# Performance work log

Measured on AMD Instinct MI355X. Metric: run time of the kernel, lower is better.

## Reference

```python
import jax, jax.numpy as jnp
import numpy as np

# B batch, N seq (n_vec), V vocab, D model dim, H heads, DH head dim,
# L depth, WS window size, R landmark rank, C classes
B, N, V, D, H, DH, L, WS, R, C = 4, 4096, 512, 512, 8, 64, 4, 128, 256, 10
FF = 4 * D
SCALE = DH ** -0.5


def _ln(t, g, b, eps=1e-5):
    mu = jnp.mean(t, axis=-1, keepdims=True)
    var = jnp.var(t, axis=-1, keepdims=True)
    return (t - mu) * jax.lax.rsqrt(var + eps) * g + b


def setup_inputs():
    key = jax.random.key(0)
    ks = iter(jax.random.split(key, 16))

    def w(shape, s=0.02):
        return (jax.random.normal(next(ks), shape) * s).astype(jnp.float32)

    return dict(
        x=jax.random.randint(next(ks), (B, N), 0, V, dtype=jnp.int32),
        tok_emb=w((V, D)), pos_emb=w((N, D)),
        ln1_g=jnp.ones((L, D), jnp.float32), ln1_b=jnp.zeros((L, D), jnp.float32),
        Wq=w((L, D, H * DH)), Wkv=w((L, D, 2 * H * DH)), Wp=w((L, DH, R)),
        lln_g=jnp.ones((L, DH), jnp.float32), lln_b=jnp.zeros((L, DH), jnp.float32),
        gln_g=jnp.ones((L, DH), jnp.float32), gln_b=jnp.zeros((L, DH), jnp.float32),
        Wo=w((L, H * DH, D)), bo=jnp.zeros((L, D), jnp.float32),
        ln2_g=jnp.ones((L, D), jnp.float32), ln2_b=jnp.zeros((L, D), jnp.float32),
        W1=w((L, D, FF)), b1=jnp.zeros((L, FF), jnp.float32),
        W2=w((L, FF, D)), b2=jnp.zeros((L, D), jnp.float32),
        lnf_g=jnp.ones((D,), jnp.float32), lnf_b=jnp.zeros((D,), jnp.float32),
        Wlog=w((D, V)), blog=jnp.zeros((V,), jnp.float32),
        Wfin=w((N * V, C), 0.005), bfin=jnp.zeros((C,), jnp.float32),
    )


def _forward(x, tok_emb, pos_emb, ln1_g, ln1_b, Wq, Wkv, Wp, lln_g, lln_b,
             gln_g, gln_b, Wo, bo, ln2_g, ln2_b, W1, b1, W2, b2,
             lnf_g, lnf_b, Wlog, blog, Wfin, bfin):
    h = tok_emb[x] + pos_emb[None, :, :]  # [B,N,D]
    nw = N // WS
    for l in range(L):
        # ---- PreNorm Long-Short attention ----
        y = _ln(h, ln1_g[l], ln1_b[l])
        q = (y @ Wq[l]).reshape(B, N, H, DH).transpose(0, 2, 1, 3) * SCALE  # [B,H,N,DH]
        kv = (y @ Wkv[l]).reshape(B, N, 2, H, DH).transpose(2, 0, 3, 1, 4)
        k, v = kv[0], kv[1]  # [B,H,N,DH]
        # dynamic low-rank landmark projection: softmax over the sequence dim
        p = jax.nn.softmax(jnp.einsum('bhnd,dr->bhnr', k, Wp[l]), axis=2)
        gk = _ln(jnp.einsum('bhnr,bhnd->bhrd', p, k), gln_g[l], gln_b[l])  # [B,H,R,DH]
        gv = _ln(jnp.einsum('bhnr,bhnd->bhrd', p, v), gln_g[l], gln_b[l])
        # DualLN on the short-range (local window) keys/values
        lk = _ln(k, lln_g[l], lln_b[l]).reshape(B, H, nw, WS, DH)
        lv = _ln(v, lln_g[l], lln_b[l]).reshape(B, H, nw, WS, DH)
        lq = q.reshape(B, H, nw, WS, DH)
        sim_l = jnp.einsum('bhnwd,bhnxd->bhnwx', lq, lk)  # [B,H,nw,WS,WS]
        sim_g = jnp.einsum('bhnwd,bhrd->bhnwr', lq, gk)   # [B,H,nw,WS,R]
        attn = jax.nn.softmax(jnp.concatenate([sim_l, sim_g], axis=-1), axis=-1)
        a_l, a_g = attn[..., :WS], attn[..., WS:]
        o = (jnp.einsum('bhnwx,bhnxd->bhnwd', a_l, lv)
             + jnp.einsum('bhnwr,bhrd->bhnwd', a_g, gv))
        o = o.reshape(B, H, N, DH).transpose(0, 2, 1, 3).reshape(B, N, H * DH)
        h = h + o @ Wo[l] + bo[l]
        # ---- PreNorm FeedForward ----
        y = _ln(h, ln2_g[l], ln2_b[l])
        h = h + jax.nn.gelu(y @ W1[l] + b1[l]) @ W2[l] + b2[l]
    logits = _ln(h, lnf_g, lnf_b) @ Wlog + blog  # [B,N,V]
    # FLATTEN pooling head (dropout is identity in eval mode)
    return logits.reshape(B, N * V) @ Wfin + bfin  # [B,C]


def reference(x, tok_emb, pos_emb, ln1_g, ln1_b, Wq, Wkv, Wp, lln_g, lln_b,
              gln_g, gln_b, Wo, bo, ln2_g, ln2_b, W1, b1, W2, b2,
              lnf_g, lnf_b, Wlog, blog, Wfin, bfin):
    return _forward(x, tok_emb, pos_emb, ln1_g, ln1_b, Wq, Wkv, Wp, lln_g, lln_b,
                    gln_g, gln_b, Wo, bo, ln2_g, ln2_b, W1, b1, W2, b2,
                    lnf_g, lnf_b, Wlog, blog, Wfin, bfin)
```

## Files before the change

kernel.cpp:

```cpp
#include <hip/hip_runtime.h>
#include <hip/hip_bf16.h>

typedef unsigned short u16;
typedef __attribute__((ext_vector_type(8))) short short8;
typedef __attribute__((ext_vector_type(4))) float floatx4;

#define FLAG_GELU   1
#define FLAG_ACC    2
#define FLAG_NN     4
#define FLAG_CF32   8
#define FLAG_ATOMIC 16

__device__ __forceinline__ float bf2f(u16 u){
  union { unsigned u; float f; } c; c.u = ((unsigned)u)<<16; return c.f;
}
__device__ __forceinline__ u16 f2bf(float f){
  union { float f; unsigned u; } c; c.f = f;
  unsigned r = (c.u + 0x7fffu + ((c.u>>16)&1u))>>16;
  return (u16)r;
}
__device__ __forceinline__ float rdin(const void* base, long long idx, int flagv){
  return flagv ? ((const float*)base)[idx] : bf2f(((const u16*)base)[idx]);
}
__device__ __forceinline__ float fast_gelu(float x){
  float u = 0.7978845608028654f*(x + 0.044715f*x*x*x);
  float e = __expf(2.f*u);
  float t = 1.f - 2.f/(e+1.f);
  return 0.5f*x*(1.f+t);
}

__global__ void detect_kernel(const void* tok, int* flag){
  __shared__ int cnt;
  if(threadIdx.x==0) cnt=0;
  __syncthreads();
  float v = fabsf(bf2f(((const u16*)tok)[threadIdx.x]));
  int bad = (v < 1e3f) ? 0 : 1;
  atomicAdd(&cnt, bad);
  __syncthreads();
  if(threadIdx.x==0) *flag = (cnt>0) ? 1 : 0;
}

__global__ void cvtT_kernel(const void* src, long long off0, long long zstride, u16* __restrict__ dst,
    long long dzstride, int K, int N, const int* flag){
  __shared__ float tl[32][33];
  int fl = *flag;
  int k0 = blockIdx.x*32, n0 = blockIdx.y*32;
  long long base = off0 + (long long)blockIdx.z*zstride;
  for(int i=threadIdx.y;i<32;i+=8){
    long long idx = base + (long long)(k0+i)*N + n0 + threadIdx.x;
    tl[i][threadIdx.x] = fl ? ((const float*)src)[idx] : bf2f(((const u16*)src)[idx]);
  }
  __syncthreads();
  u16* dz = dst + (long long)blockIdx.z*dzstride;
  for(int i=threadIdx.y;i<32;i+=8)
    dz[(long long)(n0+i)*K + k0 + threadIdx.x] = f2bf(tl[threadIdx.x][i]);
}

__global__ void transposeB_kernel(const u16* __restrict__ in, u16* __restrict__ out,
    long long izs0, long long izs1, int zd, long long ozstride, int ldin, int ldout){
  __shared__ u16 tl[32][33];
  int z = blockIdx.z; int z0 = z/zd, z1 = z - z0*zd;
  const u16* ip = in + z0*izs0 + z1*izs1;
  u16* op = out + (long long)z*ozstride;
  int r0 = blockIdx.x*32, c0 = blockIdx.y*32;
  for(int i=threadIdx.y;i<32;i+=8)
    tl[i][threadIdx.x] = ip[(long long)(r0+i)*ldin + c0 + threadIdx.x];
  __syncthreads();
  for(int i=threadIdx.y;i<32;i+=8)
    op[(long long)(c0+i)*ldout + r0 + threadIdx.x] = tl[threadIdx.x][i];
}

__global__ __launch_bounds__(256) void zerof_kernel(float* p, int n){
  int i = blockIdx.x*256 + threadIdx.x;
  if(i<n) p[i]=0.f;
}

struct GemmP {
  const u16* A; const u16* B; float* Cf; u16* Ch;
  const void* bias; int biasOff; const int* dflag;
  int K, lda, ldb, ldc;
  long long sA0,sA1,sA2,sB0,sB1,sB2,sC0,sC1,sC2;
  int d0,d1; float alpha; int flags; int ksplit;
};

__global__ __launch_bounds__(256) void gemm_kernel(GemmP p){
  __shared__ __align__(16) u16 As[64][40];
  __shared__ __align__(16) u16 Bs[64][40];
  int z = blockIdx.z;
  int i0 = z / p.d0; int rem = z - i0*p.d0; int i1 = rem / p.d1; int i2 = rem - i1*p.d1;
  const u16* A  = p.A + i0*p.sA0 + i1*p.sA1 + i2*p.sA2;
  const u16* Bp = p.B + i0*p.sB0 + i1*p.sB1 + i2*p.sB2;
  long long cb = i0*p.sC0 + i1*p.sC1 + i2*p.sC2;
  int kbeg = 0, kend = p.K;
  if(p.ksplit){ kbeg = i1*p.ksplit; kend = kbeg + p.ksplit; }
  int m0 = blockIdx.x*64, n0 = blockIdx.y*64;
  int t = threadIdx.x, lane = t&63, wave = t>>6;
  int wm = (wave>>1)*32, wn = (wave&1)*32;
  int quad = lane>>4, l16 = lane&15;
  floatx4 zero4 = {0.f,0.f,0.f,0.f};
  floatx4 acc00=zero4, acc01=zero4, acc10=zero4, acc11=zero4;
  int sr = t>>2, sc = (t&3)*8;
  int bkr = t>>3, bnc = (t&7)*8;
  bool nn = (p.flags & FLAG_NN);
  for(int k0=kbeg;k0<kend;k0+=32){
    uint4 av = *(const uint4*)(A + (long long)(m0+sr)*p.lda + (k0+sc));
    uint4 bv;
    if(nn) bv = *(const uint4*)(Bp + (long long)(k0+bkr)*p.ldb + (n0+bnc));
    else   bv = *(const uint4*)(Bp + (long long)(n0+sr)*p.ldb + (k0+sc));
    *(uint4*)&As[sr][sc] = av;
    if(nn){
      u16 tmp[8]; *(uint4*)tmp = bv;
      #pragma unroll
      for(int j=0;j<8;j++) Bs[bnc+j][bkr] = tmp[j];
    } else {
      *(uint4*)&Bs[sr][sc] = bv;
    }
    __syncthreads();
    short8 a0 = *(const short8*)&As[wm+l16][quad*8];
    short8 a1 = *(const short8*)&As[wm+16+l16][quad*8];
    short8 b0 = *(const short8*)&Bs[wn+l16][quad*8];
    short8 b1 = *(const short8*)&Bs[wn+16+l16][quad*8];
    acc00 = __builtin_amdgcn_mfma_f32_16x16x32_bf16(a0,b0,acc00,0,0,0);
    acc01 = __builtin_amdgcn_mfma_f32_16x16x32_bf16(a0,b1,acc01,0,0,0);
    acc10 = __builtin_amdgcn_mfma_f32_16x16x32_bf16(a1,b0,acc10,0,0,0);
    acc11 = __builtin_amdgcn_mfma_f32_16x16x32_bf16(a1,b1,acc11,0,0,0);
    __syncthreads();
  }
  int flagv = p.bias ? *p.dflag : 0;
  #pragma unroll
  for(int mi=0;mi<2;mi++){
    #pragma unroll
    for(int ni=0;ni<2;ni++){
      floatx4 a = (mi==0)?((ni==0)?acc00:acc01):((ni==0)?acc10:acc11);
      int cg = n0 + wn + ni*16 + l16;
      float bv_ = p.bias ? rdin(p.bias, (long long)p.biasOff + cg, flagv) : 0.f;
      #pragma unroll
      for(int e=0;e<4;e++){
        int rg = m0 + wm + mi*16 + quad*4 + e;
        float v = a[e]*p.alpha + bv_;
        if(p.flags & FLAG_GELU) v = fast_gelu(v);
        long long ci = cb + (long long)rg*p.ldc + cg;
        if(p.flags & FLAG_ATOMIC){
          atomicAdd(&p.Cf[ci], v);
        } else if(p.flags & FLAG_CF32){
          float o2 = v; if(p.flags&FLAG_ACC) o2 += p.Cf[ci];
          p.Cf[ci] = o2;
        } else {
          float o2 = v; if(p.flags&FLAG_ACC) o2 += bf2f(p.Ch[ci]);
          p.Ch[ci] = f2bf(o2);
        }
      }
    }
  }
}

struct Gemm128P {
  const u16* A; const u16* B; float* Cf; u16* Ch;
  const void* bias; int biasOff; const int* dflag;
  int K, lda, ldb, ldc; float alpha; int flags;
};

template<int BM>
__global__ __launch_bounds__(512) void gemm2ph_kernel(Gemm128P p){
  constexpr int NA   = BM/64;
  constexpr int HH   = BM/2;
  constexpr int MI   = HH/16;
  constexpr int ABUF = BM*64;
  constexpr int LDSZ = (BM==256) ? 69632 : 49152;
  __shared__ __align__(16) u16 lds[LDSZ];
  u16* As = lds;
  u16* Bs = lds + 2*ABUF;
  int m0 = blockIdx.x*BM, n0 = blockIdx.y*256;
  int t = threadIdx.x, lane = t&63, wave = t>>6;
  int quad = lane>>4, l16 = lane&15;
  int wr = wave>>2, wc = wave&3;
  int rowA = t>>3, colk = (t&7)*8;
  const u16* Asrc[NA];
  const u16* Bsrc[4];
  #pragma unroll
  for(int q=0;q<NA;q++) Asrc[q] = p.A + (long long)(m0 + q*64 + rowA)*p.lda + colk;
  #pragma unroll
  for(int q=0;q<4;q++)  Bsrc[q] = p.B + (long long)(n0 + q*64 + rowA)*p.ldb + colk;
  int nk = p.K >> 6;
  floatx4 acc[MI][4] = {};

  auto stage = [&](int buf, int k0){
    #pragma unroll
    for(int q=0;q<NA;q++)
      __builtin_amdgcn_global_load_lds(
        (const __attribute__((address_space(1))) unsigned int*)(Asrc[q] + k0),
        (__attribute__((address_space(3))) unsigned int*)(As + buf*ABUF + q*4096 + wave*512),
        16, 0, 0);
    #pragma unroll
    for(int q=0;q<4;q++)
      __builtin_amdgcn_global_load_lds(
        (const __attribute__((address_space(1))) unsigned int*)(Bsrc[q] + k0),
        (__attribute__((address_space(3))) unsigned int*)(Bs + buf*16384 + q*4096 + wave*512),
        16, 0, 0);
  };

  stage(0, 0);
  __syncthreads();
  for(int kt=0; kt<nk; ++kt){
    int cur = kt&1;
    if(kt+1 < nk) stage(cur^1, (kt+1)*64);
    const u16* Ab = As + cur*ABUF;
    const u16* Bb = Bs + cur*16384;
    #pragma unroll
    for(int ks=0; ks<2; ks++){
      short8 a[MI], b[4];
      #pragma unroll
      for(int i=0;i<MI;i++)
        a[i] = *(const short8*)&Ab[(wr*HH + i*16 + l16)*64 + ks*32 + quad*8];
      #pragma unroll
      for(int j=0;j<4;j++)
        b[j] = *(const short8*)&Bb[(wc*64 + j*16 + l16)*64 + ks*32 + quad*8];
      #pragma unroll
      for(int i=0;i<MI;i++)
        #pragma unroll
        for(int j=0;j<4;j++)
          acc[i][j] = __builtin_amdgcn_mfma_f32_16x16x32_bf16(a[i], b[j], acc[i][j],0,0,0);
    }
    __syncthreads();
  }

  int flagv = p.bias ? *p.dflag : 0;
  if(!(p.flags & FLAG_CF32)){
    u16* Ct = lds + wave*(HH*68);
    #pragma unroll
    for(int j=0;j<4;j++){
      int cg = n0 + wc*64 + j*16 + l16;
      float bv_ = p.bias ? rdin(p.bias, (long long)p.biasOff + cg, flagv) : 0.f;
      #pragma unroll
      for(int i=0;i<MI;i++){
        #pragma unroll
        for(int e=0;e<4;e++){
          float v = acc[i][j][e]*p.alpha + bv_;
          if(p.flags & FLAG_GELU) v = fast_gelu(v);
          Ct[(i*16 + quad*4 + e)*68 + j*16 + l16] = f2bf(v);
        }
      }
    }
    int rsub = lane>>3, csub = (lane&7)*8;
    #pragma unroll
    for(int rr=0; rr<HH/8; rr++){
      int row = rr*8 + rsub;
      uint4 v = *(const uint4*)&Ct[row*68 + csub];
      *(uint4*)(p.Ch + (long long)(m0 + wr*HH + row)*p.ldc + (n0 + wc*64 + csub)) = v;
    }
  } else {
    #pragma unroll
    for(int j=0;j<4;j++){
      int cg = n0 + wc*64 + j*16 + l16;
      float bv_ = p.bias ? rdin(p.bias, (long long)p.biasOff + cg, flagv) : 0.f;
      #pragma unroll
      for(int i=0;i<MI;i++){
        #pragma unroll
        for(int e=0;e<4;e++){
          int rg = m0 + wr*HH + i*16 + quad*4 + e;
          float v = acc[i][j][e]*p.alpha + bv_;
          if(p.flags & FLAG_GELU) v = fast_gelu(v);
          long long ci = (long long)rg*p.ldc + cg;
          float o2 = v; if(p.flags&FLAG_ACC) o2 += p.Cf[ci];
          p.Cf[ci] = o2;
        }
      }
    }
  }
}

struct AttnP {
  const u16* q;
  const u16* k;
  const u16* gk;
  const u16* vT;
  const u16* gvT;
  u16* o;
};

__global__ __launch_bounds__(256) void attn_kernel(AttnP p){
  __shared__ __align__(16) u16 S[32*392];
  __shared__ float ssum[32];
  const int SST = 392;
  int qb = blockIdx.x;
  int bh = blockIdx.y;
  int b = bh>>3, hh = bh&7;
  int w = qb>>2;
  int t = threadIdx.x, lane = t&63, wave = t>>6;
  int quad = lane>>4, l16 = lane&15;
  int mbase = qb*32;
  short8 aq[2][2];
  #pragma unroll
  for(int mt=0;mt<2;mt++)
    #pragma unroll
    for(int kc=0;kc<2;kc++)
      aq[mt][kc] = *(const short8*)(p.q + ((long long)b*4096 + mbase + mt*16 + l16)*512 + hh*64 + kc*32 + quad*8);
  #pragma unroll
  for(int i=0;i<6;i++){
    int ct = wave*6 + i;
    short8 bf0, bf1;
    if(ct<8){
      const u16* kr = p.k + ((long long)b*4096 + w*128 + ct*16 + l16)*1024 + hh*64;
      bf0 = *(const short8*)(kr + quad*8);
      bf1 = *(const short8*)(kr + 32 + quad*8);
    } else {
      const u16* gr = p.gk + ((long long)bh*256 + (ct-8)*16 + l16)*64;
      bf0 = *(const short8*)(gr + quad*8);
      bf1 = *(const short8*)(gr + 32 + quad*8);
    }
    #pragma unroll
    for(int mt=0;mt<2;mt++){
      floatx4 acc = {0.f,0.f,0.f,0.f};
      acc = __builtin_amdgcn_mfma_f32_16x16x32_bf16(aq[mt][0], bf0, acc,0,0,0);
      acc = __builtin_amdgcn_mfma_f32_16x16x32_bf16(aq[mt][1], bf1, acc,0,0,0);
      #pragma unroll
      for(int e=0;e<4;e++)
        S[(mt*16 + quad*4 + e)*SST + ct*16 + l16] = f2bf(acc[e]);
    }
  }
  __syncthreads();
  {
    int r = t>>3, seg = t&7;
    u16* Srow = S + r*SST + seg*48;
    u16 buf[48];
    #pragma unroll
    for(int it=0; it<6; it++)
      *(uint4*)(buf + it*8) = *(const uint4*)(Srow + it*8);
    float mmax = -3.4e38f;
    #pragma unroll
    for(int j=0;j<48;j++) mmax = fmaxf(mmax, bf2f(buf[j]));
    mmax = fmaxf(mmax, __shfl_xor(mmax, 1));
    mmax = fmaxf(mmax, __shfl_xor(mmax, 2));
    mmax = fmaxf(mmax, __shfl_xor(mmax, 4));
    float s = 0.f;
    #pragma unroll
    for(int j=0;j<48;j++){ float e_ = __expf(bf2f(buf[j]) - mmax); s += e_; buf[j] = f2bf(e_); }
    #pragma unroll
    for(int it=0; it<6; it++)
      *(uint4*)(Srow + it*8) = *(const uint4*)(buf + it*8);
    s += __shfl_xor(s, 1);
    s += __shfl_xor(s, 2);
    s += __shfl_xor(s, 4);
    if(seg==0) ssum[r] = 1.f/s;
  }
  __syncthreads();
  int dt = wave;
  floatx4 oacc[2] = {};
  for(int kc=0; kc<12; kc++){
    short8 ap0 = *(const short8*)(S + (l16)*SST + kc*32 + quad*8);
    short8 ap1 = *(const short8*)(S + (16 + l16)*SST + kc*32 + quad*8);
    short8 bv;
    if(kc<4)
      bv = *(const short8*)(p.vT + (long long)bh*262144 + (dt*16+l16)*4096 + w*128 + kc*32 + quad*8);
    else
      bv = *(const short8*)(p.gvT + (long long)bh*16384 + (dt*16+l16)*256 + (kc-4)*32 + quad*8);
    oacc[0] = __builtin_amdgcn_mfma_f32_16x16x32_bf16(ap0, bv, oacc[0],0,0,0);
    oacc[1] = __builtin_amdgcn_mfma_f32_16x16x32_bf16(ap1, bv, oacc[1],0,0,0);
  }
  #pragma unroll
  for(int mt=0;mt<2;mt++){
    #pragma unroll
    for(int e=0;e<4;e++){
      int row = mt*16 + quad*4 + e;
      float inv = ssum[row];
      p.o[((long long)b*4096 + mbase + row)*512 + hh*64 + dt*16 + l16] = f2bf(oacc[mt][e]*inv);
    }
  }
}

__global__ __launch_bounds__(256) void embed_kernel(const int* __restrict__ x, const void* tok,
    const void* pos, float* __restrict__ h, const int* flag){
  int i = blockIdx.x*256 + threadIdx.x;
  int flagv = *flag;
  int d = i & 511;
  int n = (i>>9) & 4095;
  int bn = i>>9;
  int tid2 = x[bn];
  h[i] = rdin(tok, (long long)tid2*512 + d, flagv) + rdin(pos, (long long)n*512 + d, flagv);
}

__global__ __launch_bounds__(256) void ln512_kernel(const float* __restrict__ h,
    const void* g, const void* b, int goff, u16* __restrict__ y, const int* flag){
  int row = blockIdx.x;
  int flagv = *flag;
  const float* hr = h + (size_t)row*512;
  int t = threadIdx.x;
  float x0 = hr[t], x1 = hr[t+256];
  float s1 = x0+x1, s2 = x0*x0+x1*x1;
  for(int o=32;o>0;o>>=1){ s1 += __shfl_down(s1,o,64); s2 += __shfl_down(s2,o,64); }
  __shared__ float sh1[4], sh2[4];
  int wv=t>>6, ln=t&63;
  if(ln==0){ sh1[wv]=s1; sh2[wv]=s2; }
  __syncthreads();
  float st = sh1[0]+sh1[1]+sh1[2]+sh1[3];
  float qt = sh2[0]+sh2[1]+sh2[2]+sh2[3];
  float mu = st*(1.f/512.f);
  float var = qt*(1.f/512.f) - mu*mu;
  float inv = rsqrtf(var+1e-5f);
  u16* yr = y + (size_t)row*512;
  yr[t]     = f2bf((x0-mu)*inv*rdin(g,goff+t,flagv)     + rdin(b,goff+t,flagv));
  yr[t+256] = f2bf((x1-mu)*inv*rdin(g,goff+t+256,flagv) + rdin(b,goff+t+256,flagv));
}

__global__ __launch_bounds__(256) void ln64_kernel(const u16* __restrict__ in, const float* __restrict__ inF,
    u16* __restrict__ out, const void* g, const void* b, int goff,
    long long s0, long long s1v, long long s2v, int d0, int d1, const int* flag){
  int r = blockIdx.x*4 + (threadIdx.x>>6);
  int ln = threadIdx.x&63;
  int flagv = *flag;
  int i0 = r/d0; int rem = r - i0*d0; int i1 = rem/d1; int i2 = rem - i1*d1;
  long long off = i0*s0 + i1*s1v + i2*s2v;
  float x = inF ? inF[off+ln] : bf2f(in[off + ln]);
  float s = x, sq = x*x;
  for(int o=32;o>0;o>>=1){ s += __shfl_down(s,o,64); sq += __shfl_down(sq,o,64); }
  s = __shfl(s,0,64); sq = __shfl(sq,0,64);
  float mu = s*(1.f/64.f), var = sq*(1.f/64.f)-mu*mu;
  float inv = rsqrtf(var+1e-5f);
  out[off + ln] = f2bf((x-mu)*inv*rdin(g,goff+ln,flagv) + rdin(b,goff+ln,flagv));
}

__global__ __launch_bounds__(256) void softmax4096_kernel(u16* __restrict__ p){
  u16* pr = p + (size_t)blockIdx.x*4096;
  int t = threadIdx.x;
  u16 tmp[16];
  *(uint4*)tmp     = *(const uint4*)(pr + t*16);
  *(uint4*)(tmp+8) = *(const uint4*)(pr + t*16 + 8);
  float xs[16]; float m=-3.4e38f;
  #pragma unroll
  for(int i=0;i<16;i++){ xs[i]=bf2f(tmp[i]); m=fmaxf(m,xs[i]); }
  for(int o=32;o>0;o>>=1) m = fmaxf(m, __shfl_down(m,o,64));
  __shared__ float sm[4]; __shared__ float sv[4];
  int wv=t>>6, ln=t&63;
  if(ln==0) sm[wv]=m;
  __syncthreads();
  m = fmaxf(fmaxf(sm[0],sm[1]),fmaxf(sm[2],sm[3]));
  float s=0;
  #pragma unroll
  for(int i=0;i<16;i++){ xs[i]=__expf(xs[i]-m); s+=xs[i]; }
  for(int o=32;o>0;o>>=1) s += __shfl_down(s,o,64);
  if(ln==0) sv[wv]=s;
  __syncthreads();
  s = sv[0]+sv[1]+sv[2]+sv[3];
  float inv = 1.f/s;
  #pragma unroll
  for(int i=0;i<16;i++) tmp[i]=f2bf(xs[i]*inv);
  *(uint4*)(pr + t*16)     = *(uint4*)tmp;
  *(uint4*)(pr + t*16 + 8) = *(uint4*)(tmp+8);
}

__global__ void zero40_kernel(float* p){ if(threadIdx.x<40) p[threadIdx.x]=0.f; }

__global__ __launch_bounds__(256) void head_kernel(const float* __restrict__ logits,
    const void* wfin, float* __restrict__ part, const int* flag){
  int b = blockIdx.x>>7, chunk = blockIdx.x&127;
  int flagv = *flag;
  const float* lr = logits + (size_t)b*2097152 + (size_t)chunk*16384;
  float acc[10];
  #pragma unroll
  for(int c=0;c<10;c++) acc[c]=0.f;
  for(int j=threadIdx.x;j<16384;j+=256){
    float lv_ = lr[j];
    long long wb = (long long)(chunk*16384 + j)*10;
    if(flagv){
      const float* w = (const float*)wfin + wb;
      #pragma unroll
      for(int c=0;c<10;c++) acc[c] += lv_*w[c];
    } else {
      const u16* w = (const u16*)wfin + wb;
      #pragma unroll
      for(int c=0;c<10;c++) acc[c] += lv_*bf2f(w[c]);
    }
  }
  __shared__ float red[4];
  int wv=threadIdx.x>>6, ln=threadIdx.x&63;
  for(int c=0;c<10;c++){
    float v=acc[c];
    for(int o=32;o>0;o>>=1) v+=__shfl_down(v,o,64);
    __syncthreads();
    if(ln==0) red[wv]=v;
    __syncthreads();
    if(threadIdx.x==0) atomicAdd(&part[b*10+c], red[0]+red[1]+red[2]+red[3]);
  }
}

__global__ void fin_kernel(const float* __restrict__ part, const void* bfin, void* out, const int* flag){
  int i=threadIdx.x;
  int flagv = *flag;
  if(i<40){
    float r = part[i] + rdin(bfin, i%10, flagv);
    if(flagv) ((float*)out)[i] = r;
    else      ((u16*)out)[i]   = f2bf(r);
  }
}

static const size_t OFF_H    = 0;
static const size_t OFF_Y    = 33554432;
static const size_t OFF_GKF  = 33554432;
static const size_t OFF_GVF  = 35651584;
static const size_t OFF_Q    = 50331648;
static const size_t OFF_KV   = 67108864;
static const size_t OFF_GK   = 100663296;
static const size_t OFF_GV   = 101711872;
static const size_t OFF_BIG  = 102760448;
static const size_t OFF_KT   = 169869312;
static const size_t OFF_VT   = 186646528;
static const size_t OFF_WTP  = 203423744;
static const size_t OFF_WQT  = 203554816;
static const size_t OFF_WKVT = 204079104;
static const size_t OFF_WOT  = 205127680;
static const size_t OFF_W1T  = 205651968;
static const size_t OFF_W2T  = 207749120;
static const size_t OFF_PART = 209846272;
static const size_t OFF_FLAG = 209846528;
static const size_t WS_NEED  = 209846784;

static inline GemmP mkg(const void*A,const void*B,void*C,const void*bias,int biasOff,const int* dflag,
  int K,int lda,int ldb,int ldc,
  long long a0,long long a1,long long a2,long long b0,long long b1,long long b2,
  long long c0,long long c1,long long c2,int d0,int d1,float alpha,int flags,int ksplit){
  GemmP p; p.A=(const u16*)A; p.B=(const u16*)B;
  p.Cf=(float*)C; p.Ch=(u16*)C; p.bias=bias; p.biasOff=biasOff; p.dflag=dflag;
  p.K=K;p.lda=lda;p.ldb=ldb;p.ldc=ldc;
  p.sA0=a0;p.sA1=a1;p.sA2=a2;p.sB0=b0;p.sB1=b1;p.sB2=b2;p.sC0=c0;p.sC1=c1;p.sC2=c2;
  p.d0=d0;p.d1=d1;p.alpha=alpha;p.flags=flags;p.ksplit=ksplit; return p;
}
static inline Gemm128P mk128(const void*A,const void*B,void*C,const void*bias,int biasOff,const int* dflag,
  int K,int lda,int ldb,int ldc,float alpha,int flags){
  Gemm128P p; p.A=(const u16*)A; p.B=(const u16*)B;
  p.Cf=(float*)C; p.Ch=(u16*)C; p.bias=bias; p.biasOff=biasOff; p.dflag=dflag;
  p.K=K;p.lda=lda;p.ldb=ldb;p.ldc=ldc;p.alpha=alpha;p.flags=flags; return p;
}

extern "C" void kernel_launch(void* const* d_in, const int* in_sizes, int n_in,
                              void* d_out, int out_size, void* d_ws, size_t ws_size,
                              hipStream_t stream){
  (void)in_sizes;(void)n_in;(void)out_size;
  if(ws_size < WS_NEED) return;
  const int*  x    = (const int*)d_in[0];
  const void* tok  = d_in[1];
  const void* pos  = d_in[2];
  const void* ln1g = d_in[3];
  const void* ln1b = d_in[4];
  const void* Wq   = d_in[5];
  const void* Wkv  = d_in[6];
  const void* Wp   = d_in[7];
  const void* llng = d_in[8];
  const void* llnb = d_in[9];
  const void* glng = d_in[10];
  const void* glnb = d_in[11];
  const void* Wo   = d_in[12];
  const void* bo   = d_in[13];
  const void* ln2g = d_in[14];
  const void* ln2b = d_in[15];
  const void* W1   = d_in[16];
  const void* b1   = d_in[17];
  const void* W2   = d_in[18];
  const void* b2   = d_in[19];
  const void* lnfg = d_in[20];
  const void* lnfb = d_in[21];
  const void* Wlog = d_in[22];
  const void* blog = d_in[23];
  const void* Wfin = d_in[24];
  const void* bfin = d_in[25];

  char* ws = (char*)d_ws;
  float* h    = (float*)(ws + OFF_H);
  u16* y      = (u16*)(ws + OFF_Y);
  u16* ob     = (u16*)(ws + OFF_Y);
  float* gkF  = (float*)(ws + OFF_GKF);
  float* gvF  = (float*)(ws + OFF_GVF);
  u16* qb     = (u16*)(ws + OFF_Q);
  u16* kv     = (u16*)(ws + OFF_KV);
  u16* gk     = (u16*)(ws + OFF_GK);
  u16* gv     = (u16*)(ws + OFF_GV);
  u16* big    = (u16*)(ws + OFF_BIG);
  float* bigf = (float*)(ws + OFF_BIG);
  u16* kT     = (u16*)(ws + OFF_KT);
  u16* gvT    = (u16*)(ws + OFF_KT);
  u16* vT     = (u16*)(ws + OFF_VT);
  u16* wTp    = (u16*)(ws + OFF_WTP);
  u16* sWqT   = (u16*)(ws + OFF_WQT);
  u16* sWkvT  = (u16*)(ws + OFF_WKVT);
  u16* sWoT   = (u16*)(ws + OFF_WOT);
  u16* sW1T   = (u16*)(ws + OFF_W1T);
  u16* sW2T   = (u16*)(ws + OFF_W2T);
  float* part = (float*)(ws + OFF_PART);
  int* flag   = (int*)(ws + OFF_FLAG);

  dim3 tb(32,8);
  detect_kernel<<<dim3(1),dim3(256),0,stream>>>(tok, flag);
  cvtT_kernel<<<dim3(2,8,4),tb,0,stream>>>(Wp, 0, 16384, wTp, 16384, 64, 256, flag);
  embed_kernel<<<dim3(32768),dim3(256),0,stream>>>(x, tok, pos, h, flag);

  for(int l=0;l<4;l++){
    cvtT_kernel<<<dim3(16,16,1),tb,0,stream>>>(Wq,  (long long)l*262144,  0, sWqT,  0, 512, 512,  flag);
    cvtT_kernel<<<dim3(16,32,1),tb,0,stream>>>(Wkv, (long long)l*524288,  0, sWkvT, 0, 512, 1024, flag);
    cvtT_kernel<<<dim3(16,16,1),tb,0,stream>>>(Wo,  (long long)l*262144,  0, sWoT,  0, 512, 512,  flag);
    cvtT_kernel<<<dim3(16,64,1),tb,0,stream>>>(W1,  (long long)l*1048576, 0, sW1T,  0, 512, 2048, flag);
    cvtT_kernel<<<dim3(64,16,1),tb,0,stream>>>(W2,  (long long)l*1048576, 0, sW2T,  0, 2048, 512, flag);

    ln512_kernel<<<dim3(16384),dim3(256),0,stream>>>(h, ln1g, ln1b, l*512, y, flag);
    { Gemm128P p = mk128(y, sWqT, qb, nullptr,0,flag, 512,512,512,512, 0.125f, 0);
      gemm2ph_kernel<128><<<dim3(128,2),512,0,stream>>>(p); }
    { Gemm128P p = mk128(y, sWkvT, kv, nullptr,0,flag, 512,512,512,1024, 1.f, 0);
      gemm2ph_kernel<256><<<dim3(64,4),512,0,stream>>>(p); }
    zerof_kernel<<<dim3(4096),dim3(256),0,stream>>>(gkF, 1048576);
    { GemmP p = mkg(wTp + (size_t)l*16384, kv, big, nullptr,0,flag, 64,64,1024,4096,
        0,0,0, 4194304LL,64,0, 8388608LL,1048576LL,0, 8,1, 1.f, 0, 0);
      gemm_kernel<<<dim3(4,64,32),256,0,stream>>>(p); }
    softmax4096_kernel<<<dim3(8192),dim3(256),0,stream>>>(big);
    transposeB_kernel<<<dim3(128,2,32),tb,0,stream>>>(kv,     kT, 4194304LL,64,8, 262144LL, 1024, 4096);
    transposeB_kernel<<<dim3(128,2,32),tb,0,stream>>>(kv+512, vT, 4194304LL,64,8, 262144LL, 1024, 4096);
    { GemmP p = mkg(big, kT, gkF, nullptr,0,flag, 4096,4096,4096,64,
        1048576LL,0,0, 262144LL,0,0, 16384LL,0,0, 8,1, 1.f, FLAG_CF32|FLAG_ATOMIC, 512);
      gemm_kernel<<<dim3(4,1,256),256,0,stream>>>(p); }
    { GemmP p = mkg(big, vT, gvF, nullptr,0,flag, 4096,4096,4096,64,
        1048576LL,0,0, 262144LL,0,0, 16384LL,0,0, 8,1, 1.f, FLAG_CF32|FLAG_ATOMIC, 512);
      gemm_kernel<<<dim3(4,1,256),256,0,stream>>>(p); }
    ln64_kernel<<<dim3(2048),dim3(256),0,stream>>>(gk, gkF, gk, glng, glnb, l*64, 64,1,1, 1,1, flag);
    ln64_kernel<<<dim3(2048),dim3(256),0,stream>>>(gv, gvF, gv, glng, glnb, l*64, 64,1,1, 1,1, flag);
    ln64_kernel<<<dim3(32768),dim3(256),0,stream>>>(kv,     nullptr, kv,     llng, llnb, l*64, 4194304LL,64,1024, 32768,4096, flag);
    ln64_kernel<<<dim3(32768),dim3(256),0,stream>>>(kv+512, nullptr, kv+512, llng, llnb, l*64, 4194304LL,64,1024, 32768,4096, flag);
    transposeB_kernel<<<dim3(128,2,32),tb,0,stream>>>(kv+512, vT, 4194304LL,64,8, 262144LL, 1024, 4096);
    transposeB_kernel<<<dim3(8,2,32),tb,0,stream>>>(gv, gvT, 16384LL,0,1, 16384LL, 64, 256);
    { AttnP ap; ap.q=qb; ap.k=kv; ap.gk=gk; ap.vT=vT; ap.gvT=gvT; ap.o=ob;
      attn_kernel<<<dim3(128,32),256,0,stream>>>(ap); }
    { Gemm128P p = mk128(ob, sWoT, h, bo,l*512,flag, 512,512,512,512, 1.f, FLAG_ACC|FLAG_CF32);
      gemm2ph_kernel<128><<<dim3(128,2),512,0,stream>>>(p); }
    ln512_kernel<<<dim3(16384),dim3(256),0,stream>>>(h, ln2g, ln2b, l*512, y, flag);
    { Gemm128P p = mk128(y, sW1T, big, b1,l*2048,flag, 512,512,512,2048, 1.f, FLAG_GELU);
      gemm2ph_kernel<256><<<dim3(64,8),512,0,stream>>>(p); }
    { Gemm128P p = mk128(big, sW2T, h, b2,l*512,flag, 2048,2048,2048,512, 1.f, FLAG_ACC|FLAG_CF32);
      gemm2ph_kernel<128><<<dim3(128,2),512,0,stream>>>(p); }
  }
  ln512_kernel<<<dim3(16384),dim3(256),0,stream>>>(h, lnfg, lnfb, 0, y, flag);
  cvtT_kernel<<<dim3(16,16,1),tb,0,stream>>>(Wlog, 0, 0, sWqT, 0, 512, 512, flag);
  { Gemm128P p = mk128(y, sWqT, bigf, blog,0,flag, 512,512,512,512, 1.f, FLAG_CF32);
    gemm2ph_kernel<128><<<dim3(128,2),512,0,stream>>>(p); }
  zero40_kernel<<<dim3(1),dim3(64),0,stream>>>(part);
  head_kernel<<<dim3(512),dim3(256),0,stream>>>(bigf, Wfin, part, flag);
  fin_kernel<<<dim3(1),dim3(64),0,stream>>>(part, bfin, d_out, flag);
}
```

Before: 2.476 ms.

## Swizzle GEMM LDS layout, drop k/v transposes, widen head kernel loads

Applies an XOR swizzle to the LDS column index in the two-phase MFMA GEMM so fragment reads avoid bank conflicts. Removes the two explicit k/v transposes before the landmark projection GEMMs. Those GEMMs now read kv directly in NN mode, with the split-K index moved to the innermost batch dimension. Rewrites the classification head to process pairs of logits per thread with vectorized weight loads and twice as many blocks. The combined changes carry correctness risk in the stride and ksplit reindexing.

Result: faster. 2.347 ms (-5.2%).

```diff
diff --git a/kernel.cpp b/kernel.cpp
--- a/kernel.cpp
+++ b/kernel.cpp
@@ -92,7 +92,7 @@
   const u16* Bp = p.B + i0*p.sB0 + i1*p.sB1 + i2*p.sB2;
   long long cb = i0*p.sC0 + i1*p.sC1 + i2*p.sC2;
   int kbeg = 0, kend = p.K;
-  if(p.ksplit){ kbeg = i1*p.ksplit; kend = kbeg + p.ksplit; }
+  if(p.ksplit){ kbeg = i2*p.ksplit; kend = kbeg + p.ksplit; }
   int m0 = blockIdx.x*64, n0 = blockIdx.y*64;
   int t = threadIdx.x, lane = t&63, wave = t>>6;
   int wm = (wave>>1)*32, wn = (wave&1)*32;
@@ -174,7 +174,8 @@
   int t = threadIdx.x, lane = t&63, wave = t>>6;
   int quad = lane>>4, l16 = lane&15;
   int wr = wave>>2, wc = wave&3;
-  int rowA = t>>3, colk = (t&7)*8;
+  int rowA = t>>3;
+  int colk = (((t&7) ^ (rowA&7)))*8;
   const u16* Asrc[NA];
   const u16* Bsrc[4];
   #pragma unroll
@@ -201,6 +202,7 @@
 
   stage(0, 0);
   __syncthreads();
+  int sw = l16&7;
   for(int kt=0; kt<nk; ++kt){
     int cur = kt&1;
     if(kt+1 < nk) stage(cur^1, (kt+1)*64);
@@ -211,10 +213,10 @@
       short8 a[MI], b[4];
       #pragma unroll
       for(int i=0;i<MI;i++)
-        a[i] = *(const short8*)&Ab[(wr*HH + i*16 + l16)*64 + ks*32 + quad*8];
+        a[i] = *(const short8*)&Ab[(wr*HH + i*16 + l16)*64 + ((((ks<<2)|quad) ^ sw)<<3)];
       #pragma unroll
       for(int j=0;j<4;j++)
-        b[j] = *(const short8*)&Bb[(wc*64 + j*16 + l16)*64 + ks*32 + quad*8];
+        b[j] = *(const short8*)&Bb[(wc*64 + j*16 + l16)*64 + ((((ks<<2)|quad) ^ sw)<<3)];
       #pragma unroll
       for(int i=0;i<MI;i++)
         #pragma unroll
@@ -452,23 +454,33 @@
 
 __global__ __launch_bounds__(256) void head_kernel(const float* __restrict__ logits,
     const void* wfin, float* __restrict__ part, const int* flag){
-  int b = blockIdx.x>>7, chunk = blockIdx.x&127;
+  int b = blockIdx.x>>8, chunk = blockIdx.x&255;
   int flagv = *flag;
-  const float* lr = logits + (size_t)b*2097152 + (size_t)chunk*16384;
+  const float* lr = logits + (size_t)b*2097152 + (size_t)chunk*8192;
+  long long jbase = (long long)chunk*8192;
   float acc[10];
   #pragma unroll
   for(int c=0;c<10;c++) acc[c]=0.f;
-  for(int j=threadIdx.x;j<16384;j+=256){
-    float lv_ = lr[j];
-    long long wb = (long long)(chunk*16384 + j)*10;
+  for(int it=0; it<16; ++it){
+    int jp = it*256 + threadIdx.x;
+    float2 lv = *(const float2*)(lr + jp*2);
+    long long wrow = (jbase + (long long)jp*2)*10;
     if(flagv){
-      const float* w = (const float*)wfin + wb;
-      #pragma unroll
-      for(int c=0;c<10;c++) acc[c] += lv_*w[c];
+      const float* w = (const float*)wfin + wrow;
+      #pragma unroll
+      for(int c=0;c<10;c++) acc[c] += lv.x*w[c] + lv.y*w[c+10];
     } else {
-      const u16* w = (const u16*)wfin + wb;
-      #pragma unroll
-      for(int c=0;c<10;c++) acc[c] += lv_*bf2f(w[c]);
+      const unsigned* wu = (const unsigned*)((const u16*)wfin + wrow);
+      unsigned wd[10];
+      #pragma unroll
+      for(int k2=0;k2<10;k2++) wd[k2] = wu[k2];
+      #pragma unroll
+      for(int c=0;c<10;c++){
+        unsigned lo = wd[c>>1], hi = wd[5+(c>>1)];
+        float w0 = bf2f((u16)((c&1)? (lo>>16) : (lo&0xffffu)));
+        float w1 = bf2f((u16)((c&1)? (hi>>16) : (hi&0xffffu)));
+        acc[c] += lv.x*w0 + lv.y*w1;
+      }
     }
   }
   __shared__ float red[4];
@@ -575,7 +587,6 @@
   u16* gv     = (u16*)(ws + OFF_GV);
   u16* big    = (u16*)(ws + OFF_BIG);
   float* bigf = (float*)(ws + OFF_BIG);
-  u16* kT     = (u16*)(ws + OFF_KT);
   u16* gvT    = (u16*)(ws + OFF_KT);
   u16* vT     = (u16*)(ws + OFF_VT);
   u16* wTp    = (u16*)(ws + OFF_WTP);
@@ -609,13 +620,13 @@
         0,0,0, 4194304LL,64,0, 8388608LL,1048576LL,0, 8,1, 1.f, 0, 0);
       gemm_kernel<<<dim3(4,64,32),256,0,stream>>>(p); }
     softmax4096_kernel<<<dim3(8192),dim3(256),0,stream>>>(big);
-    transposeB_kernel<<<dim3(128,2,32),tb,0,stream>>>(kv,     kT, 4194304LL,64,8, 262144LL, 1024, 4096);
-    transposeB_kernel<<<dim3(128,2,32),tb,0,stream>>>(kv+512, vT, 4194304LL,64,8, 262144LL, 1024, 4096);
-    { GemmP p = mkg(big, kT, gkF, nullptr,0,flag, 4096,4096,4096,64,
-        1048576LL,0,0, 262144LL,0,0, 16384LL,0,0, 8,1, 1.f, FLAG_CF32|FLAG_ATOMIC, 512);
+    { GemmP p = mkg(big, kv, gkF, nullptr,0,flag, 4096,4096,1024,64,
+        8388608LL,1048576LL,0, 4194304LL,64,0, 131072LL,16384LL,0, 64,8, 1.f,
+        FLAG_CF32|FLAG_ATOMIC|FLAG_NN, 512);
       gemm_kernel<<<dim3(4,1,256),256,0,stream>>>(p); }
-    { GemmP p = mkg(big, vT, gvF, nullptr,0,flag, 4096,4096,4096,64,
-        1048576LL,0,0, 262144LL,0,0, 16384LL,0,0, 8,1, 1.f, FLAG_CF32|FLAG_ATOMIC, 512);
+    { GemmP p = mkg(big, kv+512, gvF, nullptr,0,flag, 4096,4096,1024,64,
+        8388608LL,1048576LL,0, 4194304LL,64,0, 131072LL,16384LL,0, 64,8, 1.f,
+        FLAG_CF32|FLAG_ATOMIC|FLAG_NN, 512);
       gemm_kernel<<<dim3(4,1,256),256,0,stream>>>(p); }
     ln64_kernel<<<dim3(2048),dim3(256),0,stream>>>(gk, gkF, gk, glng, glnb, l*64, 64,1,1, 1,1, flag);
     ln64_kernel<<<dim3(2048),dim3(256),0,stream>>>(gv, gvF, gv, glng, glnb, l*64, 64,1,1, 1,1, flag);
@@ -638,6 +649,6 @@
   { Gemm128P p = mk128(y, sWqT, bigf, blog,0,flag, 512,512,512,512, 1.f, FLAG_CF32);
     gemm2ph_kernel<128><<<dim3(128,2),512,0,stream>>>(p); }
   zero40_kernel<<<dim3(1),dim3(64),0,stream>>>(part);
-  head_kernel<<<dim3(512),dim3(256),0,stream>>>(bigf, Wfin, part, flag);
+  head_kernel<<<dim3(1024),dim3(256),0,stream>>>(bigf, Wfin, part, flag);
   fin_kernel<<<dim3(1),dim3(64),0,stream>>>(part, bfin, d_out, flag);
 }
```
